# Optimization experiments

Hardware: AMD Instinct MI355X
Metric: run time of the kernel (lower is better)

Reference implementation:

```python
import jax, jax.numpy as jnp
import numpy as np
from jax import lax

THRE = 0.01
K_SIZE = 5
C_SIGMA = 1.0
VOXEL = 0.4          # args['voxel_size'][0] -> discrete_ratio
DOWNSAMPLE = 4       # args['downsample_rate']


def gaussian_kernel(k=K_SIZE, sigma=C_SIGMA):
    c = k // 2
    gx, gy = np.mgrid[-c:k - c, -c:k - c]
    g = 1.0 / (2.0 * np.pi * sigma) * np.exp(-(gx ** 2 + gy ** 2) / (2.0 * sigma ** 2))
    return jnp.asarray(g, dtype=jnp.float32)


def affine_grid(theta, H, W):
    # theta: [N,2,3]; matches F.affine_grid(align_corners=False)
    dt = theta.dtype
    xs = (jnp.arange(W, dtype=dt) + 0.5) * (2.0 / W) - 1.0
    ys = (jnp.arange(H, dtype=dt) + 0.5) * (2.0 / H) - 1.0
    xg, yg = jnp.meshgrid(xs, ys)                      # [H,W]
    base = jnp.stack([xg, yg, jnp.ones_like(xg)], -1)  # [H,W,3]
    return jnp.einsum('hwk,nck->nhwc', base, theta)    # [N,H,W,2] (x_s, y_s)


def grid_sample_bilinear(src, grid):
    # src [N,C,H,W], grid [N,H,W,2] in [-1,1]; bilinear, zeros padding, align_corners=False
    N, C, H, W = src.shape
    x = ((grid[..., 0] + 1.0) * W - 1.0) * 0.5
    y = ((grid[..., 1] + 1.0) * H - 1.0) * 0.5
    x0f = jnp.floor(x)
    y0f = jnp.floor(y)
    wx1 = x - x0f
    wy1 = y - y0f

    def sample_one(src_n, x0f_n, y0f_n, wx1_n, wy1_n):
        x0 = x0f_n.astype(jnp.int32)
        y0 = y0f_n.astype(jnp.int32)

        def gather(ix, iy):
            valid = ((ix >= 0) & (ix < W) & (iy >= 0) & (iy < H)).astype(src.dtype)
            ixc = jnp.clip(ix, 0, W - 1)
            iyc = jnp.clip(iy, 0, H - 1)
            return src_n[:, iyc, ixc] * valid[None]    # [C,H,W]

        g00 = gather(x0, y0)
        g01 = gather(x0 + 1, y0)
        g10 = gather(x0, y0 + 1)
        g11 = gather(x0 + 1, y0 + 1)
        wx0 = 1.0 - wx1_n
        wy0 = 1.0 - wy1_n
        return (g00 * (wx0 * wy0)[None] + g01 * (wx1_n * wy0)[None]
                + g10 * (wx0 * wy1_n)[None] + g11 * (wx1_n * wy1_n)[None])

    return jax.vmap(sample_one)(src, x0f, y0f, wx1, wy1)


def atten_fuse(feat):
    # feat: [N,C,H,W]; per-pixel scaled-dot-product attention over agents, keep ego row.
    N, C, H, W = feat.shape
    seq = feat.reshape(N, C, H * W).transpose(2, 0, 1)          # [HW, N, C]
    q0 = seq[:, 0, :]                                           # ego query [HW, C]
    score = jnp.einsum('pc,pnc->pn', q0, seq) / np.sqrt(C)      # row 0 of NxN scores
    attn = jax.nn.softmax(score, axis=-1)
    ctx = jnp.einsum('pn,pnc->pc', attn, seq)                   # [HW, C]
    return ctx.T.reshape(C, H, W)


def _forward(x, psm_single, pairwise_t_matrix):
    B, L = pairwise_t_matrix.shape[:2]
    _, C, H, W = x.shape
    A = psm_single.shape[1]

    # ---- normalize 4x4 transforms to 2x3 affine matrices (as in Where2comm.forward)
    t = pairwise_t_matrix[..., :2, :][..., jnp.array([0, 1, 3])]   # [B,L,L,2,3]
    t = t.at[..., 0, 1].multiply(H / W)
    t = t.at[..., 1, 0].multiply(W / H)
    t = t.at[..., 0, 2].set(t[..., 0, 2] / (DOWNSAMPLE * VOXEL * W) * 2.0)
    t = t.at[..., 1, 2].set(t[..., 1, 2] / (DOWNSAMPLE * VOXEL * H) * 2.0)

    # ---- Communication: confidence -> gaussian smooth -> threshold mask
    conf = jnp.max(jax.nn.sigmoid(psm_single), axis=1, keepdims=True)  # [B*L,1,H,W]
    gk = gaussian_kernel()
    pad = (K_SIZE - 1) // 2
    smoothed = lax.conv_general_dilated(
        conf, gk[None, None], (1, 1), [(pad, pad), (pad, pad)],
        dimension_numbers=('NCHW', 'OIHW', 'NCHW'))
    mask = (smoothed > THRE).astype(x.dtype)                            # [B*L,1,H,W]
    mask = mask.reshape(B, L, 1, H, W)
    mask = mask.at[:, ::2].set(1.0)                                     # nodiag trick per batch
    rate = jnp.mean(jnp.sum(mask[:, 0], axis=(1, 2, 3)) / (H * W))

    # ---- mask features, warp every agent into ego frame, attention-fuse
    xm = x.reshape(B, L, C, H, W) * mask[:, :, :, :, :]                 # broadcast over C

    def fuse_scene(feat_b, t_b):
        # feat_b: [L,C,H,W]; t_b: [L,L,2,3]; ego row of transforms warps all agents to ego
        grid = affine_grid(t_b[0], H, W)                                # [L,H,W,2]
        neighbor = grid_sample_bilinear(feat_b, grid)                   # [L,C,H,W]
        return atten_fuse(neighbor)                                     # [C,H,W]

    x_fuse = jax.vmap(fuse_scene)(xm, t)                                # [B,C,H,W]
    return x_fuse, rate


def setup_inputs() -> dict:
    key = jax.random.key(0)
    B, L, C, A, H, W = 2, 5, 256, 2, 100, 252
    k1, k2, k3 = jax.random.split(key, 3)
    x = jax.random.normal(k1, (B * L, C, H, W), jnp.float32)
    psm_single = jax.random.normal(k2, (B * L, A, H, W), jnp.float32)
    # near-identity 4x4 pose transforms with small random translations (meters)
    t = jnp.tile(jnp.eye(4, dtype=jnp.float32), (B, L, L, 1, 1))
    trans = jax.random.uniform(k3, (B, L, L, 2), jnp.float32, -10.0, 10.0)
    t = t.at[..., 0, 3].set(trans[..., 0])
    t = t.at[..., 1, 3].set(trans[..., 1])
    idx = jnp.arange(L)
    t = t.at[:, idx, idx].set(jnp.eye(4, dtype=jnp.float32))  # self-transform = identity
    record_len = jnp.full((B,), L, dtype=jnp.int32)
    return {"x": x, "psm_single": psm_single, "pairwise_t_matrix": t, "record_len": record_len}


def reference(x, psm_single, pairwise_t_matrix, record_len):
    x_fuse, rate = _forward(x, psm_single, pairwise_t_matrix)
    return x_fuse
```

## Files before the change

### kernel.cpp

```cpp
#include <hip/hip_runtime.h>
#include <math.h>

#define BB 2
#define LL 5
#define CC 256
#define HH 100
#define WW 252
#define HW (HH*WW)
#define CHW (CC*HW)
#define THRE_F 0.01f

__global__ void mask_kernel(const float* __restrict__ psm, float* __restrict__ mask)
{
    int idx = blockIdx.x * blockDim.x + threadIdx.x;
    const int total = 4 * HW;
    if (idx >= total) return;
    int m = idx / HW;
    int p = idx - m * HW;
    int h = p / WW;
    int w = p - h * WW;
    int n = (m >> 1) * LL + ((m & 1) * 2 + 1);
    const float* base0 = psm + (size_t)n * 2 * HW;
    const float* base1 = base0 + HW;

    float acc = 0.0f;
#pragma unroll
    for (int i = 0; i < 5; ++i) {
        int yy = h + i - 2;
        if (yy < 0 || yy >= HH) continue;
#pragma unroll
        for (int j = 0; j < 5; ++j) {
            int xx = w + j - 2;
            if (xx < 0 || xx >= WW) continue;
            float v0 = base0[yy * WW + xx];
            float v1 = base1[yy * WW + xx];
            float v = fmaxf(v0, v1);
            float conf = 1.0f / (1.0f + expf(-v));
            double dx = (double)(j - 2), dy = (double)(i - 2);
            float g = (float)((1.0 / (2.0 * M_PI)) * exp(-0.5 * (dx * dx + dy * dy)));
            acc += g * conf;
        }
    }
    mask[idx] = (acc > THRE_F) ? 1.0f : 0.0f;
}

__global__ __launch_bounds__(256) void fuse_kernel(
    const float* __restrict__ x,
    const float* __restrict__ pt,
    const float* __restrict__ mask,
    float* __restrict__ out)
{
    int blk = blockIdx.x;
    int b   = blk / (HH * 4);
    int rem = blk - b * (HH * 4);
    int h   = rem >> 2;
    int wt  = rem & 3;

    int tid = threadIdx.x;
    int wl  = tid & 63;
    int cg  = tid >> 6;
    int w   = wt * 64 + wl;
    bool active = (w < WW);

    float xsn = (w + 0.5f) * (2.0f / WW) - 1.0f;
    float ysn = (h + 0.5f) * (2.0f / HH) - 1.0f;

    int   off[LL][4];
    float wgt[LL][4];

#pragma unroll
    for (int l = 0; l < LL; ++l) {
        const float* M = pt + (size_t)(b * LL * LL + l) * 16;
        float t00 = M[0];
        float t01 = M[1] * (100.0f / 252.0f);
        float t02 = M[3] / 403.2f * 2.0f;
        float t10 = M[4] * (252.0f / 100.0f);
        float t11 = M[5];
        float t12 = M[7] / 160.0f * 2.0f;

        float gx = t00 * xsn + t01 * ysn + t02;
        float gy = t10 * xsn + t11 * ysn + t12;
        float fx = ((gx + 1.0f) * WW - 1.0f) * 0.5f;
        float fy = ((gy + 1.0f) * HH - 1.0f) * 0.5f;
        float fx0 = floorf(fx), fy0 = floorf(fy);
        float wx1 = fx - fx0,  wy1 = fy - fy0;
        float wx0 = 1.0f - wx1, wy0 = 1.0f - wy1;
        int x0 = (int)fx0, y0 = (int)fy0;
        int x1 = x0 + 1,   y1 = y0 + 1;

        int cx0 = min(max(x0, 0), WW - 1), cx1 = min(max(x1, 0), WW - 1);
        int cy0 = min(max(y0, 0), HH - 1), cy1 = min(max(y1, 0), HH - 1);

        float vx0 = (x0 >= 0 && x0 < WW) ? 1.0f : 0.0f;
        float vx1 = (x1 >= 0 && x1 < WW) ? 1.0f : 0.0f;
        float vy0 = (y0 >= 0 && y0 < HH) ? 1.0f : 0.0f;
        float vy1 = (y1 >= 0 && y1 < HH) ? 1.0f : 0.0f;

        float m00 = 1.0f, m01 = 1.0f, m10 = 1.0f, m11 = 1.0f;
        if (l & 1) {
            const float* mb = mask + (size_t)(b * 2 + (l >> 1)) * HW;
            m00 = mb[cy0 * WW + cx0];
            m01 = mb[cy0 * WW + cx1];
            m10 = mb[cy1 * WW + cx0];
            m11 = mb[cy1 * WW + cx1];
        }

        float act = active ? 1.0f : 0.0f;
        wgt[l][0] = wx0 * wy0 * vx0 * vy0 * m00 * act;
        wgt[l][1] = wx1 * wy0 * vx1 * vy0 * m01 * act;
        wgt[l][2] = wx0 * wy1 * vx0 * vy1 * m10 * act;
        wgt[l][3] = wx1 * wy1 * vx1 * vy1 * m11 * act;

        int nbase = (b * LL + l) * CHW;
        off[l][0] = nbase + cy0 * WW + cx0;
        off[l][1] = nbase + cy0 * WW + cx1;
        off[l][2] = nbase + cy1 * WW + cx0;
        off[l][3] = nbase + cy1 * WW + cx1;
    }

    float part[LL] = {0.f, 0.f, 0.f, 0.f, 0.f};
    for (int c = cg; c < CC; c += 4) {
        int coff = c * HW;
        float f0 = wgt[0][0] * x[off[0][0] + coff]
                 + wgt[0][1] * x[off[0][1] + coff]
                 + wgt[0][2] * x[off[0][2] + coff]
                 + wgt[0][3] * x[off[0][3] + coff];
        part[0] += f0 * f0;
#pragma unroll
        for (int l = 1; l < LL; ++l) {
            float fl = wgt[l][0] * x[off[l][0] + coff]
                     + wgt[l][1] * x[off[l][1] + coff]
                     + wgt[l][2] * x[off[l][2] + coff]
                     + wgt[l][3] * x[off[l][3] + coff];
            part[l] += f0 * fl;
        }
    }

    __shared__ float sred[4][LL][64];
#pragma unroll
    for (int l = 0; l < LL; ++l) sred[cg][l][wl] = part[l];
    __syncthreads();

    __shared__ float sattn[LL][64];
    if (tid < 64) {
        float sc[LL];
        float mx = -1e30f;
#pragma unroll
        for (int l = 0; l < LL; ++l) {
            float s = (sred[0][l][wl] + sred[1][l][wl]
                     + sred[2][l][wl] + sred[3][l][wl]) * 0.0625f;
            sc[l] = s;
            mx = fmaxf(mx, s);
        }
        float denom = 0.0f;
#pragma unroll
        for (int l = 0; l < LL; ++l) { sc[l] = expf(sc[l] - mx); denom += sc[l]; }
        float inv = 1.0f / denom;
#pragma unroll
        for (int l = 0; l < LL; ++l) sattn[l][wl] = sc[l] * inv;
    }
    __syncthreads();

    float a0 = sattn[0][wl], a1 = sattn[1][wl], a2 = sattn[2][wl],
          a3 = sattn[3][wl], a4 = sattn[4][wl];

    int obase = b * CHW + h * WW + w;
    for (int c = cg; c < CC; c += 4) {
        int coff = c * HW;
        float ctx;
        {
            float fl = wgt[0][0] * x[off[0][0] + coff]
                     + wgt[0][1] * x[off[0][1] + coff]
                     + wgt[0][2] * x[off[0][2] + coff]
                     + wgt[0][3] * x[off[0][3] + coff];
            ctx = a0 * fl;
        }
        {
            float fl = wgt[1][0] * x[off[1][0] + coff]
                     + wgt[1][1] * x[off[1][1] + coff]
                     + wgt[1][2] * x[off[1][2] + coff]
                     + wgt[1][3] * x[off[1][3] + coff];
            ctx += a1 * fl;
        }
        {
            float fl = wgt[2][0] * x[off[2][0] + coff]
                     + wgt[2][1] * x[off[2][1] + coff]
                     + wgt[2][2] * x[off[2][2] + coff]
                     + wgt[2][3] * x[off[2][3] + coff];
            ctx += a2 * fl;
        }
        {
            float fl = wgt[3][0] * x[off[3][0] + coff]
                     + wgt[3][1] * x[off[3][1] + coff]
                     + wgt[3][2] * x[off[3][2] + coff]
                     + wgt[3][3] * x[off[3][3] + coff];
            ctx += a3 * fl;
        }
        {
            float fl = wgt[4][0] * x[off[4][0] + coff]
                     + wgt[4][1] * x[off[4][1] + coff]
                     + wgt[4][2] * x[off[4][2] + coff]
                     + wgt[4][3] * x[off[4][3] + coff];
            ctx += a4 * fl;
        }
        if (active) out[obase + coff] = ctx;
    }
}

extern "C" void kernel_launch(void* const* d_in, const int* in_sizes, int n_in,
                              void* d_out, int out_size, void* d_ws, size_t ws_size,
                              hipStream_t stream)
{
    const float* x   = (const float*)d_in[0];
    const float* psm = (const float*)d_in[1];
    const float* pt  = (const float*)d_in[2];
    float* out  = (float*)d_out;
    float* mask = (float*)d_ws;

    {
        int total = 4 * HW;
        int blocks = (total + 255) / 256;
        mask_kernel<<<blocks, 256, 0, stream>>>(psm, mask);
    }
    {
        int blocks = BB * HH * 4;
        fuse_kernel<<<blocks, 256, 0, stream>>>(x, pt, mask, out);
    }
}
```

Baseline: 540.4 us.

## Split fuse kernel into score and output passes with channel-split grid and paired loads

```diff
diff --git a/kernel.cpp b/kernel.cpp
--- a/kernel.cpp
+++ b/kernel.cpp
@@ -10,11 +10,24 @@
 #define CHW (CC*HW)
 #define THRE_F 0.01f
 
+__device__ const float GW[5][5] = {
+    {0.002915024f, 0.013064233f, 0.021539279f, 0.013064233f, 0.002915024f},
+    {0.013064233f, 0.058549832f, 0.096532353f, 0.058549832f, 0.013064233f},
+    {0.021539279f, 0.096532353f, 0.159154943f, 0.096532353f, 0.021539279f},
+    {0.013064233f, 0.058549832f, 0.096532353f, 0.058549832f, 0.013064233f},
+    {0.002915024f, 0.013064233f, 0.021539279f, 0.013064233f, 0.002915024f},
+};
+
+__device__ __forceinline__ float2 ld2(const float* p) {
+    float2 v;
+    __builtin_memcpy(&v, p, sizeof(float2));
+    return v;
+}
+
 __global__ void mask_kernel(const float* __restrict__ psm, float* __restrict__ mask)
 {
     int idx = blockIdx.x * blockDim.x + threadIdx.x;
-    const int total = 4 * HW;
-    if (idx >= total) return;
+    if (idx >= 4 * HW) return;
     int m = idx / HW;
     int p = idx - m * HW;
     int h = p / WW;
@@ -32,41 +45,25 @@
         for (int j = 0; j < 5; ++j) {
             int xx = w + j - 2;
             if (xx < 0 || xx >= WW) continue;
-            float v0 = base0[yy * WW + xx];
-            float v1 = base1[yy * WW + xx];
-            float v = fmaxf(v0, v1);
-            float conf = 1.0f / (1.0f + expf(-v));
-            double dx = (double)(j - 2), dy = (double)(i - 2);
-            float g = (float)((1.0 / (2.0 * M_PI)) * exp(-0.5 * (dx * dx + dy * dy)));
-            acc += g * conf;
+            float v = fmaxf(base0[yy * WW + xx], base1[yy * WW + xx]);
+            acc += GW[i][j] / (1.0f + __expf(-v));
         }
     }
     mask[idx] = (acc > THRE_F) ? 1.0f : 0.0f;
 }
 
-__global__ __launch_bounds__(256) void fuse_kernel(
-    const float* __restrict__ x,
-    const float* __restrict__ pt,
-    const float* __restrict__ mask,
-    float* __restrict__ out)
-{
-    int blk = blockIdx.x;
-    int b   = blk / (HH * 4);
-    int rem = blk - b * (HH * 4);
-    int h   = rem >> 2;
-    int wt  = rem & 3;
-
-    int tid = threadIdx.x;
-    int wl  = tid & 63;
-    int cg  = tid >> 6;
-    int w   = wt * 64 + wl;
-    bool active = (w < WW);
-
+struct TapSetup {
+    int   off0[LL], off1[LL];
+    float a0[LL], b0[LL], a1[LL], b1[LL];
+};
+
+__device__ __forceinline__ void make_taps(
+    int b, int h, int w, bool active, int c0,
+    const float* __restrict__ pt, const float* __restrict__ mask, TapSetup& T)
+{
     float xsn = (w + 0.5f) * (2.0f / WW) - 1.0f;
     float ysn = (h + 0.5f) * (2.0f / HH) - 1.0f;
-
-    int   off[LL][4];
-    float wgt[LL][4];
+    float act = active ? 1.0f : 0.0f;
 
 #pragma unroll
     for (int l = 0; l < LL; ++l) {
@@ -105,105 +102,147 @@
             m11 = mb[cy1 * WW + cx1];
         }
 
-        float act = active ? 1.0f : 0.0f;
-        wgt[l][0] = wx0 * wy0 * vx0 * vy0 * m00 * act;
-        wgt[l][1] = wx1 * wy0 * vx1 * vy0 * m01 * act;
-        wgt[l][2] = wx0 * wy1 * vx0 * vy1 * m10 * act;
-        wgt[l][3] = wx1 * wy1 * vx1 * vy1 * m11 * act;
-
-        int nbase = (b * LL + l) * CHW;
-        off[l][0] = nbase + cy0 * WW + cx0;
-        off[l][1] = nbase + cy0 * WW + cx1;
-        off[l][2] = nbase + cy1 * WW + cx0;
-        off[l][3] = nbase + cy1 * WW + cx1;
-    }
-
-    float part[LL] = {0.f, 0.f, 0.f, 0.f, 0.f};
-    for (int c = cg; c < CC; c += 4) {
-        int coff = c * HW;
-        float f0 = wgt[0][0] * x[off[0][0] + coff]
-                 + wgt[0][1] * x[off[0][1] + coff]
-                 + wgt[0][2] * x[off[0][2] + coff]
-                 + wgt[0][3] * x[off[0][3] + coff];
-        part[0] += f0 * f0;
+        float w00 = wx0 * wy0 * vx0 * vy0 * m00 * act;
+        float w01 = wx1 * wy0 * vx1 * vy0 * m01 * act;
+        float w10 = wx0 * wy1 * vx0 * vy1 * m10 * act;
+        float w11 = wx1 * wy1 * vx1 * vy1 * m11 * act;
+
+        int bx = min(max(x0, 0), WW - 2);
+        int d  = x0 - bx;
+        T.a0[l] = (d == 0 ? w00 : 0.0f) + (d == -1 ? w01 : 0.0f);
+        T.b0[l] = (d == 0 ? w01 : 0.0f) + (d ==  1 ? w00 : 0.0f);
+        T.a1[l] = (d == 0 ? w10 : 0.0f) + (d == -1 ? w11 : 0.0f);
+        T.b1[l] = (d == 0 ? w11 : 0.0f) + (d ==  1 ? w10 : 0.0f);
+
+        int nbase = (b * LL + l) * CHW + c0 * HW;
+        T.off0[l] = nbase + cy0 * WW + bx;
+        T.off1[l] = nbase + cy1 * WW + bx;
+    }
+}
+
+__global__ __launch_bounds__(256) void score_kernel(
+    const float* __restrict__ x, const float* __restrict__ pt,
+    const float* __restrict__ mask, float* __restrict__ scoresP)
+{
+    int blk = blockIdx.x;
+    int cc = blk & 1;
+    int t  = blk >> 1;
+    int wt = t & 3; t >>= 2;
+    int h  = t % HH;
+    int b  = t / HH;
+
+    int tid = threadIdx.x;
+    int wl  = tid & 63;
+    int cg  = tid >> 6;
+    int w   = wt * 64 + wl;
+    bool active = (w < WW);
+    int c0 = cc * 128 + cg * 32;
+
+    TapSetup T;
+    make_taps(b, h, w, active, c0, pt, mask, T);
+
+    float s[LL] = {0.f, 0.f, 0.f, 0.f, 0.f};
+    for (int i = 0; i < 32; ++i) {
+        float2 r0[LL], r1[LL];
+#pragma unroll
+        for (int l = 0; l < LL; ++l) {
+            r0[l] = ld2(x + T.off0[l]);
+            r1[l] = ld2(x + T.off1[l]);
+        }
+        float f0 = T.a0[0] * r0[0].x + T.b0[0] * r0[0].y
+                 + T.a1[0] * r1[0].x + T.b1[0] * r1[0].y;
+        s[0] += f0 * f0;
 #pragma unroll
         for (int l = 1; l < LL; ++l) {
-            float fl = wgt[l][0] * x[off[l][0] + coff]
-                     + wgt[l][1] * x[off[l][1] + coff]
-                     + wgt[l][2] * x[off[l][2] + coff]
-                     + wgt[l][3] * x[off[l][3] + coff];
-            part[l] += f0 * fl;
-        }
+            float fl = T.a0[l] * r0[l].x + T.b0[l] * r0[l].y
+                     + T.a1[l] * r1[l].x + T.b1[l] * r1[l].y;
+            s[l] += f0 * fl;
+        }
+#pragma unroll
+        for (int l = 0; l < LL; ++l) { T.off0[l] += HW; T.off1[l] += HW; }
     }
 
     __shared__ float sred[4][LL][64];
 #pragma unroll
-    for (int l = 0; l < LL; ++l) sred[cg][l][wl] = part[l];
+    for (int l = 0; l < LL; ++l) sred[cg][l][wl] = s[l];
     __syncthreads();
 
-    __shared__ float sattn[LL][64];
-    if (tid < 64) {
-        float sc[LL];
+    if (tid < 64 && active) {
+        int p = h * WW + w;
+#pragma unroll
+        for (int l = 0; l < LL; ++l) {
+            float v = sred[0][l][wl] + sred[1][l][wl]
+                    + sred[2][l][wl] + sred[3][l][wl];
+            scoresP[((cc * BB + b) * LL + l) * HW + p] = v;
+        }
+    }
+}
+
+__global__ __launch_bounds__(256) void out_kernel(
+    const float* __restrict__ x, const float* __restrict__ pt,
+    const float* __restrict__ mask, const float* __restrict__ scoresP,
+    float* __restrict__ out)
+{
+    int blk = blockIdx.x;
+    int cc = blk & 1;
+    int t  = blk >> 1;
+    int wt = t & 3; t >>= 2;
+    int h  = t % HH;
+    int b  = t / HH;
+
+    int tid = threadIdx.x;
+    int wl  = tid & 63;
+    int cg  = tid >> 6;
+    int w   = wt * 64 + wl;
+    bool active = (w < WW);
+    int c0 = cc * 128 + cg * 32;
+
+    float a[LL];
+    if (active) {
+        int p = h * WW + w;
         float mx = -1e30f;
 #pragma unroll
         for (int l = 0; l < LL; ++l) {
-            float s = (sred[0][l][wl] + sred[1][l][wl]
-                     + sred[2][l][wl] + sred[3][l][wl]) * 0.0625f;
-            sc[l] = s;
-            mx = fmaxf(mx, s);
+            float v = (scoresP[(b * LL + l) * HW + p]
+                     + scoresP[((BB + b) * LL + l) * HW + p]) * 0.0625f;
+            a[l] = v;
+            mx = fmaxf(mx, v);
         }
         float denom = 0.0f;
 #pragma unroll
-        for (int l = 0; l < LL; ++l) { sc[l] = expf(sc[l] - mx); denom += sc[l]; }
+        for (int l = 0; l < LL; ++l) { a[l] = expf(a[l] - mx); denom += a[l]; }
         float inv = 1.0f / denom;
 #pragma unroll
-        for (int l = 0; l < LL; ++l) sattn[l][wl] = sc[l] * inv;
-    }
-    __syncthreads();
-
-    float a0 = sattn[0][wl], a1 = sattn[1][wl], a2 = sattn[2][wl],
-          a3 = sattn[3][wl], a4 = sattn[4][wl];
-
-    int obase = b * CHW + h * WW + w;
-    for (int c = cg; c < CC; c += 4) {
-        int coff = c * HW;
-        float ctx;
-        {
-            float fl = wgt[0][0] * x[off[0][0] + coff]
-                     + wgt[0][1] * x[off[0][1] + coff]
-                     + wgt[0][2] * x[off[0][2] + coff]
-                     + wgt[0][3] * x[off[0][3] + coff];
-            ctx = a0 * fl;
-        }
-        {
-            float fl = wgt[1][0] * x[off[1][0] + coff]
-                     + wgt[1][1] * x[off[1][1] + coff]
-                     + wgt[1][2] * x[off[1][2] + coff]
-                     + wgt[1][3] * x[off[1][3] + coff];
-            ctx += a1 * fl;
-        }
-        {
-            float fl = wgt[2][0] * x[off[2][0] + coff]
-                     + wgt[2][1] * x[off[2][1] + coff]
-                     + wgt[2][2] * x[off[2][2] + coff]
-                     + wgt[2][3] * x[off[2][3] + coff];
-            ctx += a2 * fl;
-        }
-        {
-            float fl = wgt[3][0] * x[off[3][0] + coff]
-                     + wgt[3][1] * x[off[3][1] + coff]
-                     + wgt[3][2] * x[off[3][2] + coff]
-                     + wgt[3][3] * x[off[3][3] + coff];
-            ctx += a3 * fl;
-        }
-        {
-            float fl = wgt[4][0] * x[off[4][0] + coff]
-                     + wgt[4][1] * x[off[4][1] + coff]
-                     + wgt[4][2] * x[off[4][2] + coff]
-                     + wgt[4][3] * x[off[4][3] + coff];
-            ctx += a4 * fl;
-        }
-        if (active) out[obase + coff] = ctx;
+        for (int l = 0; l < LL; ++l) a[l] *= inv;
+    } else {
+#pragma unroll
+        for (int l = 0; l < LL; ++l) a[l] = 0.0f;
+    }
+
+    TapSetup T;
+    make_taps(b, h, w, active, c0, pt, mask, T);
+#pragma unroll
+    for (int l = 0; l < LL; ++l) {
+        T.a0[l] *= a[l]; T.b0[l] *= a[l]; T.a1[l] *= a[l]; T.b1[l] *= a[l];
+    }
+
+    int obase = b * CHW + c0 * HW + h * WW + w;
+    for (int i = 0; i < 32; ++i) {
+        float2 r0[LL], r1[LL];
+#pragma unroll
+        for (int l = 0; l < LL; ++l) {
+            r0[l] = ld2(x + T.off0[l]);
+            r1[l] = ld2(x + T.off1[l]);
+        }
+        float ctx = 0.0f;
+#pragma unroll
+        for (int l = 0; l < LL; ++l) {
+            ctx += T.a0[l] * r0[l].x + T.b0[l] * r0[l].y
+                 + T.a1[l] * r1[l].x + T.b1[l] * r1[l].y;
+        }
+        if (active) out[obase + i * HW] = ctx;
+#pragma unroll
+        for (int l = 0; l < LL; ++l) { T.off0[l] += HW; T.off1[l] += HW; }
     }
 }
 
@@ -214,16 +253,12 @@
     const float* x   = (const float*)d_in[0];
     const float* psm = (const float*)d_in[1];
     const float* pt  = (const float*)d_in[2];
-    float* out  = (float*)d_out;
-    float* mask = (float*)d_ws;
-
-    {
-        int total = 4 * HW;
-        int blocks = (total + 255) / 256;
-        mask_kernel<<<blocks, 256, 0, stream>>>(psm, mask);
-    }
-    {
-        int blocks = BB * HH * 4;
-        fuse_kernel<<<blocks, 256, 0, stream>>>(x, pt, mask, out);
-    }
-}
+    float* out = (float*)d_out;
+
+    float* maskw  = (float*)d_ws;
+    float* scores = maskw + 4 * HW;
+
+    mask_kernel<<<(4 * HW + 255) / 256, 256, 0, stream>>>(psm, maskw);
+    score_kernel<<<BB * HH * 4 * 2, 256, 0, stream>>>(x, pt, maskw, scores);
+    out_kernel<<<BB * HH * 4 * 2, 256, 0, stream>>>(x, pt, maskw, scores, out);
+}
```

Result: faster. 512.6 us (-5.2%).
